# Kernel tuning notes

Hardware: AMD Instinct MI355X
Metric: run time of the kernel (lower is better)

## Reference

```python
import jax, jax.numpy as jnp
import numpy as np

B, N, H, N_NODE = 512, 256, 128, 50000
ALPHA, BETA, DEGREE = 0.8, 0.1, 2


def setup_inputs() -> dict:
    key = jax.random.key(0)
    k1, k2, k3 = jax.random.split(key, 3)
    inputs = jax.random.randint(k1, (B, N), 0, N_NODE, dtype=jnp.int64)
    A = jax.random.uniform(k2, (B, N, 2 * N), dtype=jnp.float32)
    emb_weight = jax.random.normal(k3, (N_NODE, H), dtype=jnp.float32)
    return {"inputs": inputs, "A": A, "emb_weight": emb_weight}


def reference(inputs, A, emb_weight):
    # embedding lookup: [B, N, H]
    hidden = emb_weight[inputs]
    n = A.shape[1]
    # merge in/out adjacency halves
    A2 = A[:, :, :n] + A[:, :, n:2 * n]
    I = jnp.eye(n, dtype=A2.dtype)
    adj = A2 + I  # add self-loops
    # symmetric renormalization D^-1/2 (A+I) D^-1/2, vectorized over batch
    row_sum = adj.sum(axis=-1)  # [B, N]
    d_inv_sqrt = jnp.power(row_sum, -0.5)
    d_inv_sqrt = jnp.where(jnp.isinf(d_inv_sqrt), 0.0, d_inv_sqrt)
    norm_adj = adj * d_inv_sqrt[:, :, None] * d_inv_sqrt[:, None, :]
    # sgc_embed == 1 mixing: alpha * norm + beta * (1 - norm) * I
    A_mix = ALPHA * norm_adj + BETA * (1.0 - norm_adj) * I
    # SGC propagation: degree rounds of batched matmul
    for _ in range(DEGREE):
        hidden = jnp.einsum('bij,bjd->bid', A_mix, hidden)
    return hidden
```

## Files before the change

kernel.cpp:

```cpp
#include <hip/hip_runtime.h>

typedef __attribute__((ext_vector_type(8))) __bf16 bf16x8;
typedef __attribute__((ext_vector_type(4))) float f32x4;
typedef __attribute__((ext_vector_type(8))) unsigned short u16x8;
typedef __attribute__((ext_vector_type(4))) unsigned short u16x4;

#define B_SZ 512
#define N_SZ 256
#define H_SZ 128

__device__ __forceinline__ float bf2f(unsigned short u) {
    unsigned int x = ((unsigned int)u) << 16;
    return __builtin_bit_cast(float, x);
}
__device__ __forceinline__ unsigned short f2bf(float f) {
    unsigned int x = __builtin_bit_cast(unsigned int, f);
    x += 0x7FFFu + ((x >> 16) & 1u);
    return (unsigned short)(x >> 16);
}

__global__ __launch_bounds__(256) void detect_kernel(const int4* __restrict__ idx4,
                                                     int* __restrict__ flag) {
    int t = blockIdx.x * 256 + threadIdx.x;
    int any = 0;
#pragma unroll
    for (int r = 0; r < 2; r++) {
        int4 v = idx4[t + r * 16384];
        any |= (v.y | v.w);
    }
    if (any) atomicOr(flag, 1);
}

__global__ __launch_bounds__(256) void rowsum_kernel(const float* __restrict__ A,
                                                     unsigned short* __restrict__ A2,
                                                     float* __restrict__ d) {
    int row = blockIdx.x * 4 + (threadIdx.x >> 6);
    int lane = threadIdx.x & 63;
    const float* p = A + (size_t)row * 512 + lane * 4;
    f32x4 vin = *(const f32x4*)p;
    f32x4 vout = *(const f32x4*)(p + 256);
    f32x4 a2 = vin + vout;
    float s = a2[0] + a2[1] + a2[2] + a2[3];
    u16x4 pk;
#pragma unroll
    for (int e = 0; e < 4; e++) pk[e] = f2bf(a2[e]);
    *(u16x4*)(A2 + (size_t)row * 256 + lane * 4) = pk;
#pragma unroll
    for (int m = 32; m >= 1; m >>= 1) s += __shfl_xor(s, m, 64);
    if (lane == 0) d[row] = 1.0f / sqrtf(s + 1.0f);
}

__global__ __launch_bounds__(256) void mix_kernel(unsigned short* __restrict__ A2,
                                                  const float* __restrict__ d) {
    int tid = threadIdx.x;
    int row = blockIdx.x * 8 + (tid >> 5);
    int b = row >> 8;
    int i = row & 255;
    int jb = (tid & 31) * 8;
    unsigned short* Ar = A2 + (size_t)row * 256 + jb;
    u16x8 v = *(const u16x8*)Ar;
    float di = d[row];
    const float* dj = d + b * 256 + jb;
    u16x8 res;
#pragma unroll
    for (int e = 0; e < 8; e++) {
        float a = bf2f(v[e]);
        bool diag = (i == jb + e);
        if (diag) a += 1.0f;
        float na = a * di * dj[e];
        float val = 0.8f * na;
        if (diag) val += 0.1f * (1.0f - na);
        res[e] = f2bf(val);
    }
    *(u16x8*)Ar = res;
}

__global__ __launch_bounds__(256) void gather_kernel(const int* __restrict__ idx,
                                                     const float* __restrict__ emb,
                                                     const int* __restrict__ flag,
                                                     unsigned short* __restrict__ outT) {
    __shared__ unsigned short tileT[128 * 72];
    int b = blockIdx.y;
    int j0 = blockIdx.x * 64;
    int tid = threadIdx.x;
    int jj = tid & 63;
    int sub0 = (tid >> 6) * 2;
    int pos = b * 256 + j0 + jj;
    int node = (flag[0] != 0) ? idx[pos] : idx[2 * pos];
    const float* erow = emb + (size_t)node * 128;
#pragma unroll
    for (int s2 = 0; s2 < 2; s2++) {
        int h0 = (sub0 + s2) * 16;
        f32x4 v0 = *(const f32x4*)(erow + h0);
        f32x4 v1 = *(const f32x4*)(erow + h0 + 4);
        f32x4 v2 = *(const f32x4*)(erow + h0 + 8);
        f32x4 v3 = *(const f32x4*)(erow + h0 + 12);
#pragma unroll
        for (int e = 0; e < 4; e++) {
            tileT[(h0 + e) * 72 + jj] = f2bf(v0[e]);
            tileT[(h0 + 4 + e) * 72 + jj] = f2bf(v1[e]);
            tileT[(h0 + 8 + e) * 72 + jj] = f2bf(v2[e]);
            tileT[(h0 + 12 + e) * 72 + jj] = f2bf(v3[e]);
        }
    }
    __syncthreads();
#pragma unroll
    for (int p = 0; p < 4; p++) {
        int h = (tid >> 3) + p * 32;
        int jc = (tid & 7) * 8;
        u16x8 v = *(const u16x8*)(&tileT[h * 72 + jc]);
        *(u16x8*)(outT + ((size_t)b * 128 + h) * 256 + j0 + jc) = v;
    }
}

__global__ __launch_bounds__(512) void gemm_fused(const unsigned short* __restrict__ Amix,
                                                  const unsigned short* __restrict__ HT,
                                                  float* __restrict__ outF) {
    __shared__ __align__(16) unsigned char Bs[65536];
    int b = blockIdx.x;
    int tid = threadIdx.x;
    int lane = tid & 63;
    int w = tid >> 6;
    int q = lane >> 4, ln = lane & 15;
    int wm = w >> 1, wn = w & 1;

    const unsigned short* Hb = HT + (size_t)b * 128 * 256;
    const unsigned short* Ab = Amix + (size_t)b * 256 * 256;

#pragma unroll
    for (int r = 0; r < 8; r++) {
        int c = tid + r * 512;
        int h = c >> 5;
        int koff = (c & 31) << 4;
        u16x8 v = *(const u16x8*)(Hb + h * 256 + (c & 31) * 8);
        int byte = ((h << 9) + koff) ^ ((h & 7) << 4);
        *(u16x8*)(Bs + byte) = v;
    }

    int arow[4], bb[4], bsw[4];
#pragma unroll
    for (int mt = 0; mt < 4; mt++) arow[mt] = wm * 64 + mt * 16 + ln;
#pragma unroll
    for (int nt = 0; nt < 4; nt++) {
        int h = wn * 64 + nt * 16 + ln;
        bb[nt] = h << 9;
        bsw[nt] = (h & 7) << 4;
    }

    f32x4 acc[4][4];
#pragma unroll
    for (int mt = 0; mt < 4; mt++)
#pragma unroll
        for (int nt = 0; nt < 4; nt++) acc[mt][nt] = f32x4{0.f, 0.f, 0.f, 0.f};

    __syncthreads();

#pragma unroll
    for (int s = 0; s < 8; s++) {
        int k0 = s * 32;
        bf16x8 af[4], bf[4];
#pragma unroll
        for (int mt = 0; mt < 4; mt++)
            af[mt] = *(const bf16x8*)(Ab + arow[mt] * 256 + k0 + q * 8);
#pragma unroll
        for (int nt = 0; nt < 4; nt++)
            bf[nt] = *(const bf16x8*)(Bs + ((bb[nt] + k0 * 2 + q * 16) ^ bsw[nt]));
#pragma unroll
        for (int mt = 0; mt < 4; mt++)
#pragma unroll
            for (int nt = 0; nt < 4; nt++)
                acc[mt][nt] = __builtin_amdgcn_mfma_f32_16x16x32_bf16(af[mt], bf[nt],
                                                                      acc[mt][nt], 0, 0, 0);
    }

    __syncthreads();

#pragma unroll
    for (int mt = 0; mt < 4; mt++)
#pragma unroll
        for (int nt = 0; nt < 4; nt++) {
            int h = wn * 64 + nt * 16 + ln;
            int i0 = wm * 64 + mt * 16 + q * 4;
            u16x4 pk;
#pragma unroll
            for (int r = 0; r < 4; r++) pk[r] = f2bf(acc[mt][nt][r]);
            int byte = ((h << 9) + (i0 << 1)) ^ ((h & 7) << 4);
            *(u16x4*)(Bs + byte) = pk;
            acc[mt][nt] = f32x4{0.f, 0.f, 0.f, 0.f};
        }

    __syncthreads();

#pragma unroll
    for (int s = 0; s < 8; s++) {
        int k0 = s * 32;
        bf16x8 af[4], bf[4];
#pragma unroll
        for (int mt = 0; mt < 4; mt++)
            af[mt] = *(const bf16x8*)(Ab + arow[mt] * 256 + k0 + q * 8);
#pragma unroll
        for (int nt = 0; nt < 4; nt++)
            bf[nt] = *(const bf16x8*)(Bs + ((bb[nt] + k0 * 2 + q * 16) ^ bsw[nt]));
#pragma unroll
        for (int mt = 0; mt < 4; mt++)
#pragma unroll
            for (int nt = 0; nt < 4; nt++)
                acc[mt][nt] = __builtin_amdgcn_mfma_f32_16x16x32_bf16(af[mt], bf[nt],
                                                                      acc[mt][nt], 0, 0, 0);
    }

#pragma unroll
    for (int mt = 0; mt < 4; mt++)
#pragma unroll
        for (int nt = 0; nt < 4; nt++) {
            int h = wn * 64 + nt * 16 + ln;
            int i0 = wm * 64 + mt * 16 + q * 4;
#pragma unroll
            for (int r = 0; r < 4; r++)
                outF[((size_t)b * 256 + i0 + r) * 128 + h] = acc[mt][nt][r];
        }
}

extern "C" void kernel_launch(void* const* d_in, const int* in_sizes, int n_in,
                              void* d_out, int out_size, void* d_ws, size_t ws_size,
                              hipStream_t stream) {
    const int* idx = (const int*)d_in[0];
    const float* A = (const float*)d_in[1];
    const float* emb = (const float*)d_in[2];
    float* out = (float*)d_out;

    char* ws = (char*)d_ws;
    int* flag = (int*)ws;
    float* d = (float*)(ws + 4096);
    unsigned short* A2 = (unsigned short*)(ws + 528384);
    unsigned short* h0T = (unsigned short*)(ws + 67637248);

    hipMemsetAsync(flag, 0, 4, stream);
    detect_kernel<<<64, 256, 0, stream>>>((const int4*)idx, flag);
    rowsum_kernel<<<B_SZ * N_SZ / 4, 256, 0, stream>>>(A, A2, d);
    mix_kernel<<<B_SZ * N_SZ / 8, 256, 0, stream>>>(A2, d);
    gather_kernel<<<dim3(4, B_SZ), 256, 0, stream>>>(idx, emb, flag, h0T);
    gemm_fused<<<B_SZ, 512, 0, stream>>>(A2, h0T, out);
}
```

Before: 475.2 us.

## Fuse rowsum, mix, gather and both GEMMs into one per-batch kernel

Replaces the rowsum, mix, gather and GEMM kernels with a single kernel per batch element. Each block reads A directly, builds the normalized bf16 mixing matrix in LDS, and keeps the A fragments in registers for both propagation rounds. The embedding gather is transposed into LDS as well. This removes the global round trips of the intermediate A2, d and transposed-hidden buffers and several launches. In exchange it uses about 129KB of LDS per block, which allows only one block per CU, and it adds register pressure from holding the A fragments and embedding vectors.

```diff
diff --git a/kernel.cpp b/kernel.cpp
--- a/kernel.cpp
+++ b/kernel.cpp
@@ -6,14 +6,12 @@
 typedef __attribute__((ext_vector_type(4))) unsigned short u16x4;
 
 #define B_SZ 512
-#define N_SZ 256
-#define H_SZ 128
-
-__device__ __forceinline__ float bf2f(unsigned short u) {
+
+static __device__ __forceinline__ float bf2f(unsigned short u) {
     unsigned int x = ((unsigned int)u) << 16;
     return __builtin_bit_cast(float, x);
 }
-__device__ __forceinline__ unsigned short f2bf(float f) {
+static __device__ __forceinline__ unsigned short f2bf(float f) {
     unsigned int x = __builtin_bit_cast(unsigned int, f);
     x += 0x7FFFu + ((x >> 16) & 1u);
     return (unsigned short)(x >> 16);
@@ -31,190 +29,157 @@
     if (any) atomicOr(flag, 1);
 }
 
-__global__ __launch_bounds__(256) void rowsum_kernel(const float* __restrict__ A,
-                                                     unsigned short* __restrict__ A2,
-                                                     float* __restrict__ d) {
-    int row = blockIdx.x * 4 + (threadIdx.x >> 6);
-    int lane = threadIdx.x & 63;
-    const float* p = A + (size_t)row * 512 + lane * 4;
-    f32x4 vin = *(const f32x4*)p;
-    f32x4 vout = *(const f32x4*)(p + 256);
-    f32x4 a2 = vin + vout;
-    float s = a2[0] + a2[1] + a2[2] + a2[3];
-    u16x4 pk;
-#pragma unroll
-    for (int e = 0; e < 4; e++) pk[e] = f2bf(a2[e]);
-    *(u16x4*)(A2 + (size_t)row * 256 + lane * 4) = pk;
-#pragma unroll
-    for (int m = 32; m >= 1; m >>= 1) s += __shfl_xor(s, m, 64);
-    if (lane == 0) d[row] = 1.0f / sqrtf(s + 1.0f);
-}
-
-__global__ __launch_bounds__(256) void mix_kernel(unsigned short* __restrict__ A2,
-                                                  const float* __restrict__ d) {
-    int tid = threadIdx.x;
-    int row = blockIdx.x * 8 + (tid >> 5);
-    int b = row >> 8;
-    int i = row & 255;
-    int jb = (tid & 31) * 8;
-    unsigned short* Ar = A2 + (size_t)row * 256 + jb;
-    u16x8 v = *(const u16x8*)Ar;
-    float di = d[row];
-    const float* dj = d + b * 256 + jb;
-    u16x8 res;
-#pragma unroll
-    for (int e = 0; e < 8; e++) {
-        float a = bf2f(v[e]);
-        bool diag = (i == jb + e);
-        if (diag) a += 1.0f;
-        float na = a * di * dj[e];
-        float val = 0.8f * na;
-        if (diag) val += 0.1f * (1.0f - na);
-        res[e] = f2bf(val);
-    }
-    *(u16x8*)Ar = res;
-}
-
-__global__ __launch_bounds__(256) void gather_kernel(const int* __restrict__ idx,
-                                                     const float* __restrict__ emb,
-                                                     const int* __restrict__ flag,
-                                                     unsigned short* __restrict__ outT) {
-    __shared__ unsigned short tileT[128 * 72];
-    int b = blockIdx.y;
-    int j0 = blockIdx.x * 64;
-    int tid = threadIdx.x;
-    int jj = tid & 63;
-    int sub0 = (tid >> 6) * 2;
-    int pos = b * 256 + j0 + jj;
-    int node = (flag[0] != 0) ? idx[pos] : idx[2 * pos];
-    const float* erow = emb + (size_t)node * 128;
-#pragma unroll
-    for (int s2 = 0; s2 < 2; s2++) {
-        int h0 = (sub0 + s2) * 16;
-        f32x4 v0 = *(const f32x4*)(erow + h0);
-        f32x4 v1 = *(const f32x4*)(erow + h0 + 4);
-        f32x4 v2 = *(const f32x4*)(erow + h0 + 8);
-        f32x4 v3 = *(const f32x4*)(erow + h0 + 12);
-#pragma unroll
-        for (int e = 0; e < 4; e++) {
-            tileT[(h0 + e) * 72 + jj] = f2bf(v0[e]);
-            tileT[(h0 + 4 + e) * 72 + jj] = f2bf(v1[e]);
-            tileT[(h0 + 8 + e) * 72 + jj] = f2bf(v2[e]);
-            tileT[(h0 + 12 + e) * 72 + jj] = f2bf(v3[e]);
-        }
-    }
-    __syncthreads();
-#pragma unroll
-    for (int p = 0; p < 4; p++) {
-        int h = (tid >> 3) + p * 32;
-        int jc = (tid & 7) * 8;
-        u16x8 v = *(const u16x8*)(&tileT[h * 72 + jc]);
-        *(u16x8*)(outT + ((size_t)b * 128 + h) * 256 + j0 + jc) = v;
-    }
-}
-
-__global__ __launch_bounds__(512) void gemm_fused(const unsigned short* __restrict__ Amix,
-                                                  const unsigned short* __restrict__ HT,
-                                                  float* __restrict__ outF) {
-    __shared__ __align__(16) unsigned char Bs[65536];
+__global__ __launch_bounds__(512) void fused_kernel(const int* __restrict__ idx,
+                                                    const float* __restrict__ A,
+                                                    const float* __restrict__ emb,
+                                                    const int* __restrict__ flag,
+                                                    float* __restrict__ outF) {
+    __shared__ __align__(16) unsigned char smem[132096];
+    float* dL = (float*)(smem + 131072);
+
     int b = blockIdx.x;
     int tid = threadIdx.x;
+    int w = tid >> 6;
     int lane = tid & 63;
-    int w = tid >> 6;
-    int q = lane >> 4, ln = lane & 15;
-    int wm = w >> 1, wn = w & 1;
-
-    const unsigned short* Hb = HT + (size_t)b * 128 * 256;
-    const unsigned short* Ab = Amix + (size_t)b * 256 * 256;
-
-#pragma unroll
-    for (int r = 0; r < 8; r++) {
-        int c = tid + r * 512;
-        int h = c >> 5;
-        int koff = (c & 31) << 4;
-        u16x8 v = *(const u16x8*)(Hb + h * 256 + (c & 31) * 8);
-        int byte = ((h << 9) + koff) ^ ((h & 7) << 4);
-        *(u16x8*)(Bs + byte) = v;
-    }
-
-    int arow[4], bb[4], bsw[4];
-#pragma unroll
-    for (int mt = 0; mt < 4; mt++) arow[mt] = wm * 64 + mt * 16 + ln;
-#pragma unroll
-    for (int nt = 0; nt < 4; nt++) {
-        int h = wn * 64 + nt * 16 + ln;
-        bb[nt] = h << 9;
-        bsw[nt] = (h & 7) << 4;
-    }
-
-    f32x4 acc[4][4];
-#pragma unroll
-    for (int mt = 0; mt < 4; mt++)
-#pragma unroll
-        for (int nt = 0; nt < 4; nt++) acc[mt][nt] = f32x4{0.f, 0.f, 0.f, 0.f};
-
-    __syncthreads();
-
+    int q = lane >> 4;
+    int ln = lane & 15;
+
+    const float* Ab = A + (size_t)b * 256 * 512;
+
+    for (int rr = 0; rr < 32; rr += 4) {
+        f32x4 va[4], vb[4];
+#pragma unroll
+        for (int u = 0; u < 4; u++) {
+            const float* p = Ab + (size_t)(w * 32 + rr + u) * 512 + lane * 4;
+            va[u] = *(const f32x4*)p;
+            vb[u] = *(const f32x4*)(p + 256);
+        }
+#pragma unroll
+        for (int u = 0; u < 4; u++) {
+            int row = w * 32 + rr + u;
+            f32x4 a2 = va[u] + vb[u];
+            u16x4 pk;
+#pragma unroll
+            for (int e = 0; e < 4; e++) pk[e] = f2bf(a2[e]);
+            int byte_ = ((row << 9) + (lane << 3)) ^ ((row & 7) << 4);
+            *(u16x4*)(smem + byte_) = pk;
+            float s = a2[0] + a2[1] + a2[2] + a2[3];
+#pragma unroll
+            for (int m = 32; m >= 1; m >>= 1) s += __shfl_xor(s, m, 64);
+            if (lane == 0) dL[row] = 1.0f / sqrtf(s + 1.0f);
+        }
+    }
+    __syncthreads();
+
+    int j = tid & 255;
+    int hh = tid >> 8;
+    int pos = b * 256 + j;
+    int node = (flag[0] != 0) ? idx[pos] : idx[2 * pos];
+    const float* erow = emb + (size_t)node * 128 + hh * 64;
+    f32x4 ev[16];
+#pragma unroll
+    for (int p = 0; p < 16; p++) ev[p] = *(const f32x4*)(erow + p * 4);
+
+    bf16x8 afr[2][8];
 #pragma unroll
     for (int s = 0; s < 8; s++) {
-        int k0 = s * 32;
-        bf16x8 af[4], bf[4];
-#pragma unroll
-        for (int mt = 0; mt < 4; mt++)
-            af[mt] = *(const bf16x8*)(Ab + arow[mt] * 256 + k0 + q * 8);
-#pragma unroll
-        for (int nt = 0; nt < 4; nt++)
-            bf[nt] = *(const bf16x8*)(Bs + ((bb[nt] + k0 * 2 + q * 16) ^ bsw[nt]));
-#pragma unroll
-        for (int mt = 0; mt < 4; mt++)
-#pragma unroll
-            for (int nt = 0; nt < 4; nt++)
-                acc[mt][nt] = __builtin_amdgcn_mfma_f32_16x16x32_bf16(af[mt], bf[nt],
-                                                                      acc[mt][nt], 0, 0, 0);
-    }
-
-    __syncthreads();
-
-#pragma unroll
-    for (int mt = 0; mt < 4; mt++)
-#pragma unroll
-        for (int nt = 0; nt < 4; nt++) {
-            int h = wn * 64 + nt * 16 + ln;
-            int i0 = wm * 64 + mt * 16 + q * 4;
+        f32x4 dc0 = *(const f32x4*)(dL + s * 32 + q * 8);
+        f32x4 dc1 = *(const f32x4*)(dL + s * 32 + q * 8 + 4);
+#pragma unroll
+        for (int mt = 0; mt < 2; mt++) {
+            int r = w * 32 + mt * 16 + ln;
+            int byte_ = ((r << 9) + s * 64 + q * 16) ^ ((r & 7) << 4);
+            u16x8 a = *(const u16x8*)(smem + byte_);
+            float dr = dL[r];
+            u16x8 o;
+#pragma unroll
+            for (int e = 0; e < 8; e++) {
+                int c = s * 32 + q * 8 + e;
+                float av = bf2f(a[e]);
+                bool diag = (r == c);
+                if (diag) av += 1.0f;
+                float na = av * dr * ((e < 4) ? dc0[e] : dc1[e - 4]);
+                float v = 0.8f * na;
+                if (diag) v += 0.1f * (1.0f - na);
+                o[e] = f2bf(v);
+            }
+            afr[mt][s] = __builtin_bit_cast(bf16x8, o);
+        }
+    }
+    __syncthreads();
+
+#pragma unroll
+    for (int p = 0; p < 16; p++) {
+#pragma unroll
+        for (int e = 0; e < 4; e++) {
+            int h = hh * 64 + p * 4 + e;
+            int byte_ = ((h << 9) + (j << 1)) ^ ((h & 7) << 4);
+            *(unsigned short*)(smem + byte_) = f2bf(ev[p][e]);
+        }
+    }
+    __syncthreads();
+
+    f32x4 acc[2][8];
+#pragma unroll
+    for (int mt = 0; mt < 2; mt++)
+#pragma unroll
+        for (int nt = 0; nt < 8; nt++) acc[mt][nt] = f32x4{0.f, 0.f, 0.f, 0.f};
+
+#pragma unroll
+    for (int s = 0; s < 8; s++) {
+        bf16x8 bfr[8];
+#pragma unroll
+        for (int nt = 0; nt < 8; nt++) {
+            int h = nt * 16 + ln;
+            int byte_ = ((h << 9) + s * 64 + q * 16) ^ ((h & 7) << 4);
+            bfr[nt] = *(const bf16x8*)(smem + byte_);
+        }
+#pragma unroll
+        for (int mt = 0; mt < 2; mt++)
+#pragma unroll
+            for (int nt = 0; nt < 8; nt++)
+                acc[mt][nt] = __builtin_amdgcn_mfma_f32_16x16x32_bf16(
+                    afr[mt][s], bfr[nt], acc[mt][nt], 0, 0, 0);
+    }
+
+#pragma unroll
+    for (int mt = 0; mt < 2; mt++)
+#pragma unroll
+        for (int nt = 0; nt < 8; nt++) {
+            int h = nt * 16 + ln;
+            int i0 = w * 32 + mt * 16 + q * 4;
             u16x4 pk;
 #pragma unroll
             for (int r = 0; r < 4; r++) pk[r] = f2bf(acc[mt][nt][r]);
-            int byte = ((h << 9) + (i0 << 1)) ^ ((h & 7) << 4);
-            *(u16x4*)(Bs + byte) = pk;
+            int byte_ = 65536 + (((h << 9) + (i0 << 1)) ^ ((h & 7) << 4));
+            *(u16x4*)(smem + byte_) = pk;
             acc[mt][nt] = f32x4{0.f, 0.f, 0.f, 0.f};
         }
-
     __syncthreads();
 
 #pragma unroll
     for (int s = 0; s < 8; s++) {
-        int k0 = s * 32;
-        bf16x8 af[4], bf[4];
-#pragma unroll
-        for (int mt = 0; mt < 4; mt++)
-            af[mt] = *(const bf16x8*)(Ab + arow[mt] * 256 + k0 + q * 8);
-#pragma unroll
-        for (int nt = 0; nt < 4; nt++)
-            bf[nt] = *(const bf16x8*)(Bs + ((bb[nt] + k0 * 2 + q * 16) ^ bsw[nt]));
-#pragma unroll
-        for (int mt = 0; mt < 4; mt++)
-#pragma unroll
-            for (int nt = 0; nt < 4; nt++)
-                acc[mt][nt] = __builtin_amdgcn_mfma_f32_16x16x32_bf16(af[mt], bf[nt],
-                                                                      acc[mt][nt], 0, 0, 0);
-    }
-
-#pragma unroll
-    for (int mt = 0; mt < 4; mt++)
-#pragma unroll
-        for (int nt = 0; nt < 4; nt++) {
-            int h = wn * 64 + nt * 16 + ln;
-            int i0 = wm * 64 + mt * 16 + q * 4;
+        bf16x8 bfr[8];
+#pragma unroll
+        for (int nt = 0; nt < 8; nt++) {
+            int h = nt * 16 + ln;
+            int byte_ = 65536 + (((h << 9) + s * 64 + q * 16) ^ ((h & 7) << 4));
+            bfr[nt] = *(const bf16x8*)(smem + byte_);
+        }
+#pragma unroll
+        for (int mt = 0; mt < 2; mt++)
+#pragma unroll
+            for (int nt = 0; nt < 8; nt++)
+                acc[mt][nt] = __builtin_amdgcn_mfma_f32_16x16x32_bf16(
+                    afr[mt][s], bfr[nt], acc[mt][nt], 0, 0, 0);
+    }
+
+#pragma unroll
+    for (int mt = 0; mt < 2; mt++)
+#pragma unroll
+        for (int nt = 0; nt < 8; nt++) {
+            int h = nt * 16 + ln;
+            int i0 = w * 32 + mt * 16 + q * 4;
 #pragma unroll
             for (int r = 0; r < 4; r++)
                 outF[((size_t)b * 256 + i0 + r) * 128 + h] = acc[mt][nt][r];
@@ -229,16 +194,9 @@
     const float* emb = (const float*)d_in[2];
     float* out = (float*)d_out;
 
-    char* ws = (char*)d_ws;
-    int* flag = (int*)ws;
-    float* d = (float*)(ws + 4096);
-    unsigned short* A2 = (unsigned short*)(ws + 528384);
-    unsigned short* h0T = (unsigned short*)(ws + 67637248);
+    int* flag = (int*)d_ws;
 
     hipMemsetAsync(flag, 0, 4, stream);
     detect_kernel<<<64, 256, 0, stream>>>((const int4*)idx, flag);
-    rowsum_kernel<<<B_SZ * N_SZ / 4, 256, 0, stream>>>(A, A2, d);
-    mix_kernel<<<B_SZ * N_SZ / 8, 256, 0, stream>>>(A2, d);
-    gather_kernel<<<dim3(4, B_SZ), 256, 0, stream>>>(idx, emb, flag, h0T);
-    gemm_fused<<<B_SZ, 512, 0, stream>>>(A2, h0T, out);
-}
+    fused_kernel<<<B_SZ, 512, 0, stream>>>(idx, A, emb, flag, out);
+}
```

Result: faster. 440.7 us (-7.2%).
